# Kernel optimization log

Hardware: AMD Instinct MI355X
Metric: run time of the kernel (lower is better)

## Reference

```python
import jax, jax.numpy as jnp
import numpy as np

C, H, V, N, T = 256, 256, 10000, 8, 256


def _residual_mlp(x, w1, b1, w2, b2, w3, b3):
    # ResidualLayerOld: relu(lin2(relu(lin1(x)))) + x, then final Linear
    h = jax.nn.relu(x @ w1 + b1)
    h = jax.nn.relu(h @ w2 + b2) + x
    return h @ w3 + b3


def setup_inputs() -> dict:
    key = jax.random.key(0)
    ks = jax.random.split(key, 16)
    p = lambda k, shape: jax.random.normal(k, shape, jnp.float32) * 0.02
    return dict(
        text=jax.random.randint(ks[0], (N, T), 0, V),
        mask=jnp.ones((N, T), dtype=bool),
        lengths=jnp.full((N,), T - 1, dtype=jnp.int32),  # full-length sequences
        start_emb=jax.random.normal(ks[1], (C, H), jnp.float32),
        state_emb=jax.random.normal(ks[2], (C, H), jnp.float32),
        preterminal_emb=jax.random.normal(ks[3], (C, H), jnp.float32),
        start_w1=p(ks[4], (H, H)), start_b1=jnp.zeros((H,), jnp.float32),
        start_w2=p(ks[5], (H, H)), start_b2=jnp.zeros((H,), jnp.float32),
        start_w3=p(ks[6], (H, 1)), start_b3=jnp.zeros((1,), jnp.float32),
        trans_w1=p(ks[7], (H, H)), trans_b1=jnp.zeros((H,), jnp.float32),
        trans_w2=p(ks[8], (H, H)), trans_b2=jnp.zeros((H,), jnp.float32),
        trans_w3=p(ks[9], (H, C)), trans_b3=jnp.zeros((C,), jnp.float32),
        term_w1=p(ks[10], (H, H)), term_b1=jnp.zeros((H,), jnp.float32),
        term_w2=p(ks[11], (H, H)), term_b2=jnp.zeros((H,), jnp.float32),
        term_w3=p(ks[12], (H, V)), term_b3=jnp.zeros((V,), jnp.float32),
    )


def _score(text, mask, lengths,
           start_emb, state_emb, preterminal_emb,
           start_w1, start_b1, start_w2, start_b2, start_w3, start_b3,
           trans_w1, trans_b1, trans_w2, trans_b2, trans_w3, trans_b3,
           term_w1, term_b1, term_w2, term_b2, term_w3, term_b3):
    n, t = text.shape
    c = state_emb.shape[0]
    # start / transition / emission distributions (dropout_type == 'none')
    init = jax.nn.log_softmax(
        _residual_mlp(start_emb, start_w1, start_b1, start_w2, start_b2, start_w3, start_b3)[:, 0], -1)  # [C]
    trans = jax.nn.log_softmax(
        _residual_mlp(state_emb, trans_w1, trans_b1, trans_w2, trans_b2, trans_w3, trans_b3), -1)  # [C,C]
    log_em = jax.nn.log_softmax(
        _residual_mlp(preterminal_emb, term_w1, term_b1, term_w2, term_b2, term_w3, term_b3), -1)  # [C,V]
    obs = log_em.T[text]  # [N,T,C], log p(x_t | z=c)
    # torch_struct LinearChain.hmm edge potentials: phi[n,t,c_next,c_prev]
    phi = trans[None, None] + obs[:, 1:, :, None]  # [N,T-1,C,C]
    phi = phi.at[:, 0].add(init[None, None, :] + obs[:, 0][:, None, :])
    phi_t = jnp.swapaxes(phi, 0, 1)  # [T-1,N,C,C]

    def fwd_step(alpha, p):
        new = jax.nn.logsumexp(p + alpha[:, None, :], axis=-1)  # reduce over c_prev
        return new, new

    _, alphas = jax.lax.scan(fwd_step, jnp.zeros((n, c), phi.dtype), phi_t)  # [T-1,N,C]

    def bwd_step(beta, p):
        new = jax.nn.logsumexp(p + beta[:, :, None], axis=1)  # reduce over c_next
        return new, beta

    _, betas = jax.lax.scan(bwd_step, jnp.zeros((n, c), phi.dtype), phi_t, reverse=True)  # [T-1,N,C]

    alpha_prev = jnp.concatenate([jnp.zeros((1, n, c), phi.dtype), alphas[:-1]], 0)
    log_Z = jax.nn.logsumexp(alphas[-1], -1)  # [N]
    # edge posteriors
    log_m = alpha_prev[:, :, None, :] + phi_t + betas[:, :, :, None] - log_Z[None, :, None, None]
    marginals = jnp.swapaxes(jnp.exp(log_m), 0, 1)  # [N,T-1,C,C]

    evidence = jax.nn.logsumexp(alphas[lengths - 1, jnp.arange(n)], -1).sum()
    elbo = jnp.where(mask[:, 1:, None, None],
                     jax.lax.stop_gradient(marginals) * phi,
                     0.0).sum()
    return elbo, evidence


def reference(text, mask, lengths,
              start_emb, state_emb, preterminal_emb,
              start_w1, start_b1, start_w2, start_b2, start_w3, start_b3,
              trans_w1, trans_b1, trans_w2, trans_b2, trans_w3, trans_b3,
              term_w1, term_b1, term_w2, term_b2, term_w3, term_b3):
    elbo, evidence = _score(text, mask, lengths,
                            start_emb, state_emb, preterminal_emb,
                            start_w1, start_b1, start_w2, start_b2, start_w3, start_b3,
                            trans_w1, trans_b1, trans_w2, trans_b2, trans_w3, trans_b3,
                            term_w1, term_b1, term_w2, term_b2, term_w3, term_b3)
    return elbo, evidence
```

## Files before the change

kernel.cpp:

```cpp
#include <hip/hip_runtime.h>
#include <hip/hip_bf16.h>

#define C_ 256
#define H_ 256
#define V_ 10000
#define N_ 8
#define T_ 256
#define TM1_ 255
#define NB_ ((V_ + 31) / 32)

typedef _Float16 h2_t __attribute__((ext_vector_type(2)));
typedef _Float16 h4_t __attribute__((ext_vector_type(4)));
typedef _Float16 h8_t __attribute__((ext_vector_type(8)));
typedef float f4v __attribute__((ext_vector_type(4)));

__device__ __forceinline__ void bar_lgkm() {
  asm volatile("s_waitcnt lgkmcnt(0)\ns_barrier" ::: "memory");
}

__device__ __forceinline__ float wave_red_max(float v) {
#define DPP_MAX(ctrl) { int iv_ = __float_as_int(v); \
  int r_ = __builtin_amdgcn_update_dpp(iv_, iv_, ctrl, 0xF, 0xF, false); \
  v = fmaxf(v, __int_as_float(r_)); }
  DPP_MAX(0x111) DPP_MAX(0x112) DPP_MAX(0x114) DPP_MAX(0x118)
  DPP_MAX(0x142) DPP_MAX(0x143)
#undef DPP_MAX
  return __int_as_float(__builtin_amdgcn_readlane(__float_as_int(v), 63));
}
__device__ __forceinline__ float wave_red_sum(float v) {
#define DPP_ADD(ctrl) { \
  int r_ = __builtin_amdgcn_update_dpp(0, __float_as_int(v), ctrl, 0xF, 0xF, true); \
  v += __int_as_float(r_); }
  DPP_ADD(0x111) DPP_ADD(0x112) DPP_ADD(0x114) DPP_ADD(0x118)
  DPP_ADD(0x142) DPP_ADD(0x143)
#undef DPP_ADD
  return __int_as_float(__builtin_amdgcn_readlane(__float_as_int(v), 63));
}

__device__ __forceinline__ float block_allmax(float v, float* red) {
  v = wave_red_max(v);
  if ((threadIdx.x & 63) == 0) red[threadIdx.x >> 6] = v;
  __syncthreads();
  v = fmaxf(fmaxf(red[0], red[1]), fmaxf(red[2], red[3]));
  __syncthreads();
  return v;
}
__device__ __forceinline__ float block_allsum(float v, float* red) {
  v = wave_red_sum(v);
  if ((threadIdx.x & 63) == 0) red[threadIdx.x >> 6] = v;
  __syncthreads();
  v = (red[0] + red[1]) + (red[2] + red[3]);
  __syncthreads();
  return v;
}

__device__ __forceinline__ void mlp4(
    const float* __restrict__ emb,
    const float* __restrict__ w1, const float* __restrict__ b1,
    const float* __restrict__ w2, const float* __restrict__ b2,
    int r0, float (&e_s)[4][C_], float (&h_s)[4][C_], float (&h2_s)[4][C_]) {
  const int tid = threadIdx.x;
#pragma unroll
  for (int rr = 0; rr < 4; ++rr)
    e_s[rr][tid] = emb[(r0 + rr) * H_ + tid];
  __syncthreads();
  float bb = b1[tid];
  float a0 = bb, a1 = bb, a2 = bb, a3 = bb;
  for (int k4 = 0; k4 < H_ / 4; ++k4) {
    float4 e0 = ((const float4*)e_s[0])[k4];
    float4 e1 = ((const float4*)e_s[1])[k4];
    float4 e2 = ((const float4*)e_s[2])[k4];
    float4 e3 = ((const float4*)e_s[3])[k4];
    const float* wp = w1 + (k4 * 4) * H_ + tid;
    float wa = wp[0], wb = wp[H_], wc = wp[2 * H_], wd = wp[3 * H_];
    a0 = fmaf(e0.x, wa, a0); a0 = fmaf(e0.y, wb, a0);
    a0 = fmaf(e0.z, wc, a0); a0 = fmaf(e0.w, wd, a0);
    a1 = fmaf(e1.x, wa, a1); a1 = fmaf(e1.y, wb, a1);
    a1 = fmaf(e1.z, wc, a1); a1 = fmaf(e1.w, wd, a1);
    a2 = fmaf(e2.x, wa, a2); a2 = fmaf(e2.y, wb, a2);
    a2 = fmaf(e2.z, wc, a2); a2 = fmaf(e2.w, wd, a2);
    a3 = fmaf(e3.x, wa, a3); a3 = fmaf(e3.y, wb, a3);
    a3 = fmaf(e3.z, wc, a3); a3 = fmaf(e3.w, wd, a3);
  }
  h_s[0][tid] = fmaxf(a0, 0.f);
  h_s[1][tid] = fmaxf(a1, 0.f);
  h_s[2][tid] = fmaxf(a2, 0.f);
  h_s[3][tid] = fmaxf(a3, 0.f);
  __syncthreads();
  bb = b2[tid];
  a0 = bb; a1 = bb; a2 = bb; a3 = bb;
  for (int k4 = 0; k4 < H_ / 4; ++k4) {
    float4 e0 = ((const float4*)h_s[0])[k4];
    float4 e1 = ((const float4*)h_s[1])[k4];
    float4 e2 = ((const float4*)h_s[2])[k4];
    float4 e3 = ((const float4*)h_s[3])[k4];
    const float* wp = w2 + (k4 * 4) * H_ + tid;
    float wa = wp[0], wb = wp[H_], wc = wp[2 * H_], wd = wp[3 * H_];
    a0 = fmaf(e0.x, wa, a0); a0 = fmaf(e0.y, wb, a0);
    a0 = fmaf(e0.z, wc, a0); a0 = fmaf(e0.w, wd, a0);
    a1 = fmaf(e1.x, wa, a1); a1 = fmaf(e1.y, wb, a1);
    a1 = fmaf(e1.z, wc, a1); a1 = fmaf(e1.w, wd, a1);
    a2 = fmaf(e2.x, wa, a2); a2 = fmaf(e2.y, wb, a2);
    a2 = fmaf(e2.z, wc, a2); a2 = fmaf(e2.w, wd, a2);
    a3 = fmaf(e3.x, wa, a3); a3 = fmaf(e3.y, wb, a3);
    a3 = fmaf(e3.z, wc, a3); a3 = fmaf(e3.w, wd, a3);
  }
  h2_s[0][tid] = fmaxf(a0, 0.f) + e_s[0][tid];
  h2_s[1][tid] = fmaxf(a1, 0.f) + e_s[1][tid];
  h2_s[2][tid] = fmaxf(a2, 0.f) + e_s[2][tid];
  h2_s[3][tid] = fmaxf(a3, 0.f) + e_s[3][tid];
  __syncthreads();
}

__global__ __launch_bounds__(256) void k_start(
    const float* __restrict__ emb, const float* __restrict__ w1,
    const float* __restrict__ b1, const float* __restrict__ w2,
    const float* __restrict__ b2, const float* __restrict__ w3,
    const float* __restrict__ b3, float* __restrict__ slogit) {
  __shared__ __align__(16) float e_s[4][C_], h_s[4][C_], h2_s[4][C_];
  __shared__ float red[4];
  const int r0 = blockIdx.x * 4;
  const int tid = threadIdx.x;
  mlp4(emb, w1, b1, w2, b2, r0, e_s, h_s, h2_s);
  float w3v = w3[tid];
  float s0 = block_allsum(h2_s[0][tid] * w3v, red);
  float s1 = block_allsum(h2_s[1][tid] * w3v, red);
  float s2 = block_allsum(h2_s[2][tid] * w3v, red);
  float s3 = block_allsum(h2_s[3][tid] * w3v, red);
  if (tid == 0) {
    float bb = b3[0];
    slogit[r0 + 0] = s0 + bb;
    slogit[r0 + 1] = s1 + bb;
    slogit[r0 + 2] = s2 + bb;
    slogit[r0 + 3] = s3 + bb;
  }
}

__global__ void k_init(const float* __restrict__ slogit, float* __restrict__ initv) {
  __shared__ float red[4];
  const int tid = threadIdx.x;
  float x = slogit[tid];
  float m = block_allmax(x, red);
  float se = block_allsum(__expf(x - m), red);
  initv[tid] = x - m - __logf(se);
}

__global__ __launch_bounds__(256) void k_trans(
    const float* __restrict__ emb, const float* __restrict__ w1,
    const float* __restrict__ b1, const float* __restrict__ w2,
    const float* __restrict__ b2, const float* __restrict__ w3,
    const float* __restrict__ b3, float* __restrict__ Pf,
    float* __restrict__ PLf, float* __restrict__ PTf,
    _Float16* __restrict__ P_h, _Float16* __restrict__ PT_h) {
  __shared__ __align__(16) float e_s[4][C_], h_s[4][C_], h2_s[4][C_];
  __shared__ float red[4];
  const int r0 = blockIdx.x * 4;
  const int tid = threadIdx.x;
  mlp4(emb, w1, b1, w2, b2, r0, e_s, h_s, h2_s);
  float lb = b3[tid];
  float l0 = lb, l1 = lb, l2 = lb, l3 = lb;
  for (int k4 = 0; k4 < H_ / 4; ++k4) {
    float4 e0 = ((const float4*)h2_s[0])[k4];
    float4 e1 = ((const float4*)h2_s[1])[k4];
    float4 e2 = ((const float4*)h2_s[2])[k4];
    float4 e3 = ((const float4*)h2_s[3])[k4];
    const float* wp = w3 + (k4 * 4) * C_ + tid;
    float wa = wp[0], wb = wp[C_], wc = wp[2 * C_], wd = wp[3 * C_];
    l0 = fmaf(e0.x, wa, l0); l0 = fmaf(e0.y, wb, l0);
    l0 = fmaf(e0.z, wc, l0); l0 = fmaf(e0.w, wd, l0);
    l1 = fmaf(e1.x, wa, l1); l1 = fmaf(e1.y, wb, l1);
    l1 = fmaf(e1.z, wc, l1); l1 = fmaf(e1.w, wd, l1);
    l2 = fmaf(e2.x, wa, l2); l2 = fmaf(e2.y, wb, l2);
    l2 = fmaf(e2.z, wc, l2); l2 = fmaf(e2.w, wd, l2);
    l3 = fmaf(e3.x, wa, l3); l3 = fmaf(e3.y, wb, l3);
    l3 = fmaf(e3.z, wc, l3); l3 = fmaf(e3.w, wd, l3);
  }
  float lg[4] = {l0, l1, l2, l3};
#pragma unroll
  for (int rr = 0; rr < 4; ++rr) {
    float m = block_allmax(lg[rr], red);
    float e = __expf(lg[rr] - m);
    float se = block_allsum(e, red);
    float p = e / se;
    float tv = lg[rr] - m - __logf(se);
    const int r = r0 + rr;
    Pf[r * C_ + tid] = p;
    PLf[r * C_ + tid] = p * tv;
    PTf[tid * C_ + r] = p;
    P_h[r * C_ + tid] = (_Float16)p;
    PT_h[tid * C_ + r] = (_Float16)p;
  }
}

__global__ __launch_bounds__(256) void k_term_mlp(
    const float* __restrict__ emb, const float* __restrict__ w1,
    const float* __restrict__ b1, const float* __restrict__ w2,
    const float* __restrict__ b2, float* __restrict__ H2,
    float* __restrict__ H2T) {
  __shared__ __align__(16) float e_s[4][C_], h_s[4][C_], h2_s[4][C_];
  const int r0 = blockIdx.x * 4;
  const int tid = threadIdx.x;
  mlp4(emb, w1, b1, w2, b2, r0, e_s, h_s, h2_s);
#pragma unroll
  for (int rr = 0; rr < 4; ++rr) {
    const int r = r0 + rr;
    float v = h2_s[rr][tid];
    H2[r * H_ + tid] = v;
    H2T[tid * C_ + r] = v;
  }
}

__global__ __launch_bounds__(256) void k_term_stats(
    const float* __restrict__ H2, const float* __restrict__ w3,
    const float* __restrict__ b3, float* __restrict__ partm,
    float* __restrict__ parts) {
  __shared__ __align__(16) float w3_s[H_][32];
  __shared__ float b3_s[32];
  const int v0 = blockIdx.x * 32;
  const int tid = threadIdx.x;
  const int ncols = min(32, V_ - v0);
  for (int idx = tid; idx < H_ * 32; idx += 256) {
    int k = idx >> 5, c = idx & 31;
    w3_s[k][c] = (c < ncols) ? w3[k * V_ + v0 + c] : 0.f;
  }
  if (tid < 32) b3_s[tid] = (tid < ncols) ? b3[v0 + tid] : 0.f;
  __syncthreads();
  float acc[32];
#pragma unroll
  for (int c = 0; c < 32; ++c) acc[c] = 0.f;
  const float4* hq = (const float4*)(H2 + tid * H_);
  for (int k4 = 0; k4 < H_ / 4; ++k4) {
    float4 h = hq[k4];
    float hk[4];
    *(float4*)hk = h;
#pragma unroll
    for (int kk = 0; kk < 4; ++kk) {
      float hv = hk[kk];
      const int k = k4 * 4 + kk;
      const float4* wq = (const float4*)(&w3_s[k][0]);
#pragma unroll
      for (int c4 = 0; c4 < 8; ++c4) {
        float4 w = wq[c4];
        acc[c4 * 4 + 0] = fmaf(hv, w.x, acc[c4 * 4 + 0]);
        acc[c4 * 4 + 1] = fmaf(hv, w.y, acc[c4 * 4 + 1]);
        acc[c4 * 4 + 2] = fmaf(hv, w.z, acc[c4 * 4 + 2]);
        acc[c4 * 4 + 3] = fmaf(hv, w.w, acc[c4 * 4 + 3]);
      }
    }
  }
  float m = -1e30f;
#pragma unroll
  for (int c = 0; c < 32; ++c) {
    acc[c] += b3_s[c];
    if (c < ncols) m = fmaxf(m, acc[c]);
  }
  float se = 0.f;
#pragma unroll
  for (int c = 0; c < 32; ++c)
    if (c < ncols) se += __expf(acc[c] - m);
  partm[blockIdx.x * C_ + tid] = m;
  parts[blockIdx.x * C_ + tid] = se;
}

__global__ void k_denom(const float* __restrict__ partm,
                        const float* __restrict__ parts,
                        float* __restrict__ denom) {
  const int r = threadIdx.x;
  float m = -1e30f;
  for (int b = 0; b < NB_; ++b) m = fmaxf(m, partm[b * C_ + r]);
  float s = 0.f;
  for (int b = 0; b < NB_; ++b)
    s += parts[b * C_ + r] * __expf(partm[b * C_ + r] - m);
  denom[r] = m + __logf(s);
}

__global__ __launch_bounds__(256) void k_obs2(
    const int* __restrict__ text, const float* __restrict__ H2T,
    const float* __restrict__ w3, const float* __restrict__ b3,
    const float* __restrict__ denom, float* __restrict__ EOBS,
    float* __restrict__ Karr) {
  __shared__ __align__(16) float w_s[H_][8];
  __shared__ float redm[4][8];
  const int c = threadIdx.x;
  const int wid = c >> 6;
  const int lane = c & 63;
  const int base = blockIdx.x * 8;
  int tok[8];
#pragma unroll
  for (int i = 0; i < 8; ++i) tok[i] = text[base + i];
  float wtmp[8];
#pragma unroll
  for (int i = 0; i < 8; ++i) wtmp[i] = w3[c * V_ + tok[i]];
  float b3t[8];
#pragma unroll
  for (int i = 0; i < 8; ++i) b3t[i] = b3[tok[i]];
#pragma unroll
  for (int i = 0; i < 8; ++i) w_s[c][i] = wtmp[i];
  __syncthreads();
  float acc[8];
#pragma unroll
  for (int i = 0; i < 8; ++i) acc[i] = 0.f;
  for (int k4 = 0; k4 < H_ / 4; ++k4) {
    float hv[4];
#pragma unroll
    for (int kk = 0; kk < 4; ++kk) hv[kk] = H2T[(k4 * 4 + kk) * C_ + c];
#pragma unroll
    for (int kk = 0; kk < 4; ++kk) {
      const float4* wq = (const float4*)(&w_s[k4 * 4 + kk][0]);
      float4 wa = wq[0], wb = wq[1];
      acc[0] = fmaf(hv[kk], wa.x, acc[0]);
      acc[1] = fmaf(hv[kk], wa.y, acc[1]);
      acc[2] = fmaf(hv[kk], wa.z, acc[2]);
      acc[3] = fmaf(hv[kk], wa.w, acc[3]);
      acc[4] = fmaf(hv[kk], wb.x, acc[4]);
      acc[5] = fmaf(hv[kk], wb.y, acc[5]);
      acc[6] = fmaf(hv[kk], wb.z, acc[6]);
      acc[7] = fmaf(hv[kk], wb.w, acc[7]);
    }
  }
  float dn = denom[c];
  float obsv[8];
#pragma unroll
  for (int i = 0; i < 8; ++i) obsv[i] = acc[i] + b3t[i] - dn;
#pragma unroll
  for (int i = 0; i < 8; ++i) {
    float wm = wave_red_max(obsv[i]);
    if (lane == 0) redm[wid][i] = wm;
  }
  __syncthreads();
#pragma unroll
  for (int i = 0; i < 8; ++i) {
    float Ki = fmaxf(fmaxf(redm[0][i], redm[1][i]),
                     fmaxf(redm[2][i], redm[3][i]));
    EOBS[(base + i) * C_ + c] = __expf(obsv[i] - Ki);
    if (c == 0) Karr[base + i] = Ki;
  }
}

__global__ __launch_bounds__(256, 1) void k_scan4(
    const _Float16* __restrict__ P_h, const _Float16* __restrict__ PT_h,
    const float* __restrict__ initv, const float* __restrict__ EOBS,
    const float* __restrict__ Karr, float* __restrict__ AL,
    float* __restrict__ BL, float* __restrict__ CC, float* __restrict__ DD,
    float* __restrict__ LOGZ) {
  __shared__ __align__(16) _Float16 ubuf[2][C_];
  __shared__ float red[4];
  const int tid = threadIdx.x;
  const int wave = tid >> 6;
  const int lane = tid & 63;
  const int quad = lane >> 4;
  const int nn16 = lane & 15;
  const bool bwd = blockIdx.x >= N_;
  const int n = blockIdx.x & (N_ - 1);
  const _Float16* __restrict__ M = bwd ? PT_h : P_h;

  h8_t afrag[4][8];
#pragma unroll
  for (int mt = 0; mt < 4; ++mt) {
    const _Float16* rp = M + (size_t)((wave << 6) + (mt << 4) + nn16) * C_ + (quad << 3);
#pragma unroll
    for (int kt = 0; kt < 8; ++kt)
      afrag[mt][kt] = *(const h8_t*)(rp + (kt << 5));
  }
  const int stb = (wave << 6) + (quad << 2);

  if (!bwd) {
    float K0 = Karr[n * T_];
    f4v x0[4];
    float lmax = -1e30f;
#pragma unroll
    for (int mt = 0; mt < 4; ++mt) {
      const int st0 = stb + (mt << 4);
      f4v iv = *(const f4v*)(initv + st0);
      f4v e0 = *(const f4v*)(EOBS + (size_t)(n * T_) * C_ + st0);
#pragma unroll
      for (int r = 0; r < 4; ++r) {
        x0[mt][r] = iv[r] + __logf(e0[r]) + K0;
        lmax = fmaxf(lmax, x0[mt][r]);
      }
    }
    float wm = wave_red_max(lmax);
    if (lane == 0) red[wave] = wm;
    __syncthreads();
    float m0 = fmaxf(fmaxf(red[0], red[1]), fmaxf(red[2], red[3]));
    __syncthreads();
    float Cacc = m0;
    f4v uval[4];
#pragma unroll
    for (int mt = 0; mt < 4; ++mt) {
      const int st0 = stb + (mt << 4);
#pragma unroll
      for (int r = 0; r < 4; ++r) uval[mt][r] = __expf(x0[mt][r] - m0);
      if (nn16 == 0) {
        h4_t p;
#pragma unroll
        for (int r = 0; r < 4; ++r) p[r] = (_Float16)uval[mt][r];
        *(h4_t*)(&ubuf[0][st0]) = p;
        *(f4v*)(AL + (size_t)(0 * N_ + n) * C_ + st0) = uval[mt];
      }
    }
    if (tid == 0) CC[0 * N_ + n] = Cacc;
    float invm = 1.f, logm = 0.f;
    f4v eo_nx[4];
#pragma unroll
    for (int mt = 0; mt < 4; ++mt)
      eo_nx[mt] = *(const f4v*)(EOBS + (size_t)(n * T_ + 1) * C_ + stb + (mt << 4));
    float K_nx = Karr[n * T_ + 1];
    __syncthreads();

#pragma unroll 1
    for (int t = 0; t < TM1_; ++t) {
      const int cur = t & 1, nxt = cur ^ 1;
      f4v eo_pf[4];
      float K_pf = 0.f;
      if (t + 2 < T_) {
#pragma unroll
        for (int mt = 0; mt < 4; ++mt)
          eo_pf[mt] = *(const f4v*)(EOBS + (size_t)(n * T_ + t + 2) * C_ + stb + (mt << 4));
        K_pf = Karr[n * T_ + t + 2];
      }
      h8_t bf[8];
#pragma unroll
      for (int kt = 0; kt < 8; ++kt)
        bf[kt] = *(const h8_t*)(&ubuf[cur][(kt << 5) + (quad << 3)]);
      f4v acc[4];
#pragma unroll
      for (int mt = 0; mt < 4; ++mt) acc[mt] = (f4v){0.f, 0.f, 0.f, 0.f};
#pragma unroll
      for (int kt = 0; kt < 8; ++kt) {
#pragma unroll
        for (int mt = 0; mt < 4; ++mt)
          acc[mt] = __builtin_amdgcn_mfma_f32_16x16x32_f16(afrag[mt][kt], bf[kt], acc[mt], 0, 0, 0);
      }
      float lmx = -1e30f;
#pragma unroll
      for (int mt = 0; mt < 4; ++mt) {
#pragma unroll
        for (int r = 0; r < 4; ++r) {
          float u = acc[mt][r] * invm * eo_nx[mt][r];
          uval[mt][r] = u;
          lmx = fmaxf(lmx, u);
        }
      }
      Cacc += K_nx + logm;
      const bool resc = (t & 3) == 3;
      if (resc) {
        float wmm = wave_red_max(lmx);
        if (lane == 0) red[wave] = wmm;
      }
      if (nn16 == 0) {
#pragma unroll
        for (int mt = 0; mt < 4; ++mt) {
          const int st0 = stb + (mt << 4);
          h4_t p;
#pragma unroll
          for (int r = 0; r < 4; ++r) p[r] = (_Float16)uval[mt][r];
          *(h4_t*)(&ubuf[nxt][st0]) = p;
          *(f4v*)(AL + (size_t)((t + 1) * N_ + n) * C_ + st0) = uval[mt];
        }
      }
      if (tid == 0) CC[(t + 1) * N_ + n] = Cacc;
      bar_lgkm();
      if (resc) {
        float m = fmaxf(fmaxf(red[0], red[1]), fmaxf(red[2], red[3]));
        m = fmaxf(m, 1e-30f);
        invm = 1.f / m;
        logm = __logf(m);
      } else { invm = 1.f; logm = 0.f; }
#pragma unroll
      for (int mt = 0; mt < 4; ++mt) eo_nx[mt] = eo_pf[mt];
      K_nx = K_pf;
    }
    float s = 0.f;
#pragma unroll
    for (int mt = 0; mt < 4; ++mt)
      s += (uval[mt][0] + uval[mt][1]) + (uval[mt][2] + uval[mt][3]);
    s = wave_red_sum(s);
    if (lane == 0) red[wave] = s;
    __syncthreads();
    float S = ((red[0] + red[1]) + (red[2] + red[3])) * (1.f / 16.f);
    if (tid == 0) LOGZ[n] = __logf(S) + Cacc;
  } else {
    float Dacc = 0.f;
    f4v vval[4];
#pragma unroll
    for (int mt = 0; mt < 4; ++mt) {
      const int st0 = stb + (mt << 4);
      vval[mt] = *(const f4v*)(EOBS + ((size_t)n * T_ + TM1_) * C_ + st0);
      if (nn16 == 0) {
        h4_t p;
#pragma unroll
        for (int r = 0; r < 4; ++r) p[r] = (_Float16)vval[mt][r];
        *(h4_t*)(&ubuf[0][st0]) = p;
        f4v one = (f4v){1.f, 1.f, 1.f, 1.f};
        *(f4v*)(BL + (size_t)((TM1_ - 1) * N_ + n) * C_ + st0) = one;
      }
    }
    if (tid == 0) DD[(TM1_ - 1) * N_ + n] = 0.f;
    float K_nx = Karr[n * T_ + TM1_];
    f4v eo_nx[4];
#pragma unroll
    for (int mt = 0; mt < 4; ++mt)
      eo_nx[mt] = *(const f4v*)(EOBS + (size_t)(n * T_ + TM1_ - 1) * C_ + stb + (mt << 4));
    __syncthreads();

#pragma unroll 1
    for (int it = 0, t = TM1_ - 2; t >= 0; --t, ++it) {
      const int cur = it & 1, nxt = cur ^ 1;
      f4v eo_pf[4];
      float K_pf = 0.f;
      if (t >= 1) {
#pragma unroll
        for (int mt = 0; mt < 4; ++mt)
          eo_pf[mt] = *(const f4v*)(EOBS + (size_t)(n * T_ + t) * C_ + stb + (mt << 4));
        K_pf = Karr[n * T_ + t + 1];
      }
      float invm = 1.f, logm = 0.f;
      if ((it & 3) == 3) {
        float m = fmaxf(fmaxf(red[0], red[1]), fmaxf(red[2], red[3]));
        m = fmaxf(m, 1e-30f);
        invm = 1.f / m;
        logm = __logf(m);
      }
      h8_t bf[8];
#pragma unroll
      for (int kt = 0; kt < 8; ++kt)
        bf[kt] = *(const h8_t*)(&ubuf[cur][(kt << 5) + (quad << 3)]);
      f4v acc[4];
#pragma unroll
      for (int mt = 0; mt < 4; ++mt) acc[mt] = (f4v){0.f, 0.f, 0.f, 0.f};
#pragma unroll
      for (int kt = 0; kt < 8; ++kt) {
#pragma unroll
        for (int mt = 0; mt < 4; ++mt)
          acc[mt] = __builtin_amdgcn_mfma_f32_16x16x32_f16(afrag[mt][kt], bf[kt], acc[mt], 0, 0, 0);
      }
      Dacc += K_nx + logm;
      float lmx = -1e30f;
      f4v blv[4];
#pragma unroll
      for (int mt = 0; mt < 4; ++mt) {
#pragma unroll
        for (int r = 0; r < 4; ++r) {
          float b = acc[mt][r] * invm;
          blv[mt][r] = b;
          float v = b * eo_nx[mt][r];
          vval[mt][r] = v;
          lmx = fmaxf(lmx, v);
        }
      }
      if (((it + 1) & 3) == 3) {
        float wmm = wave_red_max(lmx);
        if (lane == 0) red[wave] = wmm;
      }
      if (nn16 == 0) {
#pragma unroll
        for (int mt = 0; mt < 4; ++mt) {
          const int st0 = stb + (mt << 4);
          h4_t p;
#pragma unroll
          for (int r = 0; r < 4; ++r) p[r] = (_Float16)vval[mt][r];
          *(h4_t*)(&ubuf[nxt][st0]) = p;
          *(f4v*)(BL + (size_t)(t * N_ + n) * C_ + st0) = blv[mt];
        }
      }
      if (tid == 0) DD[t * N_ + n] = Dacc;
      bar_lgkm();
#pragma unroll
      for (int mt = 0; mt < 4; ++mt) eo_nx[mt] = eo_pf[mt];
      K_nx = K_pf;
    }
  }
}

__global__ __launch_bounds__(256) void k_elbo(
    const float* __restrict__ Pf, const float* __restrict__ PLf,
    const float* __restrict__ PTf, const float* __restrict__ AL,
    const float* __restrict__ BL, const float* __restrict__ CC,
    const float* __restrict__ DD, const float* __restrict__ EOBS,
    const float* __restrict__ Karr, const float* __restrict__ LOGZ,
    float* __restrict__ out) {
  __shared__ __align__(16) float A_s[N_][C_];
  __shared__ __align__(16) float B_s[N_][C_];
  __shared__ float red[4];
  const int t = blockIdx.x;
  const int c = threadIdx.x;
  if (t == 0 && c == 0) {
    float s = 0.f;
#pragma unroll
    for (int nn = 0; nn < N_; ++nn) s += LOGZ[nn];
    out[1] = s;
  }
  float sc[N_], Kv[N_], cc[N_];
#pragma unroll
  for (int nn = 0; nn < N_; ++nn) {
    A_s[nn][c] = AL[(t * N_ + nn) * C_ + c];
    Kv[nn] = Karr[nn * T_ + t + 1];
    cc[nn] = CC[t * N_ + nn];
    sc[nn] = __expf(cc[nn] + DD[t * N_ + nn] + Kv[nn] - LOGZ[nn]);
  }
  __syncthreads();
  float accPA[N_], accPL[N_];
#pragma unroll
  for (int nn = 0; nn < N_; ++nn) { accPA[nn] = 0.f; accPL[nn] = 0.f; }
  const float4* pr = (const float4*)(Pf + c * C_);
  const float4* plr = (const float4*)(PLf + c * C_);
  for (int j = 0; j < C_ / 4; ++j) {
    float4 p = pr[j];
    float4 pl = plr[j];
#pragma unroll
    for (int nn = 0; nn < N_; ++nn) {
      float4 a = ((const float4*)A_s[nn])[j];
      accPA[nn] += p.x * a.x + p.y * a.y + p.z * a.z + p.w * a.w;
      accPL[nn] += pl.x * a.x + pl.y * a.y + pl.z * a.z + pl.w * a.w;
    }
  }
  float contrib = 0.f;
  float Bv[N_];
#pragma unroll
  for (int nn = 0; nn < N_; ++nn) {
    float eo = EOBS[(nn * T_ + t + 1) * C_ + c];
    float ob = __logf(eo) + Kv[nn];
    float B = eo * BL[(t * N_ + nn) * C_ + c] * sc[nn];
    Bv[nn] = B;
    contrib += B * fmaf(ob, accPA[nn], accPL[nn]);
  }
  if (t == 0) {
#pragma unroll
    for (int nn = 0; nn < N_; ++nn) B_s[nn][c] = Bv[nn];
    __syncthreads();
    const float4* ptq = (const float4*)(PTf + c * C_);
    float accPT[N_];
#pragma unroll
    for (int nn = 0; nn < N_; ++nn) accPT[nn] = 0.f;
    for (int j = 0; j < C_ / 4; ++j) {
      float4 p = ptq[j];
#pragma unroll
      for (int nn = 0; nn < N_; ++nn) {
        float4 b = ((const float4*)B_s[nn])[j];
        accPT[nn] += p.x * b.x + p.y * b.y + p.z * b.z + p.w * b.w;
      }
    }
#pragma unroll
    for (int nn = 0; nn < N_; ++nn) {
      float a0v = A_s[nn][c];
      if (a0v > 0.f)
        contrib += a0v * (__logf(a0v) + cc[nn]) * accPT[nn];
    }
  }
  contrib = wave_red_sum(contrib);
  if ((c & 63) == 0) red[c >> 6] = contrib;
  __syncthreads();
  if (c == 0) atomicAdd(out, (red[0] + red[1]) + (red[2] + red[3]));
}

extern "C" void kernel_launch(void* const* d_in, const int* in_sizes, int n_in,
                              void* d_out, int out_size, void* d_ws, size_t ws_size,
                              hipStream_t stream) {
  (void)in_sizes; (void)n_in; (void)out_size; (void)ws_size;
  const int* text = (const int*)d_in[0];
  const float* start_emb = (const float*)d_in[3];
  const float* state_emb = (const float*)d_in[4];
  const float* pre_emb   = (const float*)d_in[5];
  const float* sw1 = (const float*)d_in[6];  const float* sb1 = (const float*)d_in[7];
  const float* sw2 = (const float*)d_in[8];  const float* sb2 = (const float*)d_in[9];
  const float* sw3 = (const float*)d_in[10]; const float* sb3 = (const float*)d_in[11];
  const float* tw1 = (const float*)d_in[12]; const float* tb1 = (const float*)d_in[13];
  const float* tw2 = (const float*)d_in[14]; const float* tb2 = (const float*)d_in[15];
  const float* tw3 = (const float*)d_in[16]; const float* tb3 = (const float*)d_in[17];
  const float* ew1 = (const float*)d_in[18]; const float* eb1 = (const float*)d_in[19];
  const float* ew2 = (const float*)d_in[20]; const float* eb2 = (const float*)d_in[21];
  const float* ew3 = (const float*)d_in[22]; const float* eb3 = (const float*)d_in[23];
  float* out = (float*)d_out;

  char* p = (char*)d_ws;
  auto alloc = [&](size_t bytes) -> char* {
    char* r = p;
    p += (bytes + 255) & ~(size_t)255;
    return r;
  };
  float* slogit = (float*)alloc(C_ * 4);
  float* initv  = (float*)alloc(C_ * 4);
  float* denom  = (float*)alloc(C_ * 4);
  float* LOGZ   = (float*)alloc(N_ * 4);
  float* Pf     = (float*)alloc(C_ * C_ * 4);
  float* PLf    = (float*)alloc(C_ * C_ * 4);
  float* PTf    = (float*)alloc(C_ * C_ * 4);
  _Float16* P_h  = (_Float16*)alloc(C_ * C_ * 2);
  _Float16* PT_h = (_Float16*)alloc(C_ * C_ * 2);
  float* H2    = (float*)alloc(C_ * H_ * 4);
  float* H2T   = (float*)alloc(C_ * H_ * 4);
  float* partm = (float*)alloc(NB_ * C_ * 4);
  float* parts = (float*)alloc(NB_ * C_ * 4);
  float* EOBS  = (float*)alloc((size_t)N_ * T_ * C_ * 4);
  float* Karr  = (float*)alloc((size_t)N_ * T_ * 4);
  float* AL    = (float*)alloc((size_t)T_ * N_ * C_ * 4);
  float* BL    = (float*)alloc((size_t)TM1_ * N_ * C_ * 4);
  float* CC    = (float*)alloc((size_t)T_ * N_ * 4);
  float* DD    = (float*)alloc((size_t)TM1_ * N_ * 4);

  hipMemsetAsync(d_out, 0, 2 * sizeof(float), stream);

  k_start<<<dim3(C_ / 4), dim3(256), 0, stream>>>(start_emb, sw1, sb1, sw2, sb2, sw3, sb3, slogit);
  k_init<<<dim3(1), dim3(256), 0, stream>>>(slogit, initv);
  k_trans<<<dim3(C_ / 4), dim3(256), 0, stream>>>(state_emb, tw1, tb1, tw2, tb2, tw3, tb3,
                                                  Pf, PLf, PTf, P_h, PT_h);
  k_term_mlp<<<dim3(C_ / 4), dim3(256), 0, stream>>>(pre_emb, ew1, eb1, ew2, eb2, H2, H2T);
  k_term_stats<<<dim3(NB_), dim3(256), 0, stream>>>(H2, ew3, eb3, partm, parts);
  k_denom<<<dim3(1), dim3(256), 0, stream>>>(partm, parts, denom);
  k_obs2<<<dim3(N_ * T_ / 8), dim3(256), 0, stream>>>(text, H2T, ew3, eb3, denom, EOBS, Karr);
  k_scan4<<<dim3(2 * N_), dim3(256), 0, stream>>>(P_h, PT_h, initv, EOBS, Karr,
                                                  AL, BL, CC, DD, LOGZ);
  k_elbo<<<dim3(TM1_), dim3(256), 0, stream>>>(Pf, PLf, PTf, AL, BL, CC, DD,
                                               EOBS, Karr, LOGZ, out);
}
```

Before: 550.4 us.

## Split HMM scan across eight waves with deeper emission prefetch

After: 517.0 us. -6.1%, faster.

```diff
diff --git a/kernel.cpp b/kernel.cpp
--- a/kernel.cpp
+++ b/kernel.cpp
@@ -8,6 +8,7 @@
 #define T_ 256
 #define TM1_ 255
 #define NB_ ((V_ + 31) / 32)
+#define SW_ 8
 
 typedef _Float16 h2_t __attribute__((ext_vector_type(2)));
 typedef _Float16 h4_t __attribute__((ext_vector_type(4)));
@@ -337,16 +338,16 @@
   }
 }
 
-__global__ __launch_bounds__(256, 1) void k_scan4(
+__global__ __launch_bounds__(512, 2) void k_scan5(
     const _Float16* __restrict__ P_h, const _Float16* __restrict__ PT_h,
     const float* __restrict__ initv, const float* __restrict__ EOBS,
     const float* __restrict__ Karr, float* __restrict__ AL,
     float* __restrict__ BL, float* __restrict__ CC, float* __restrict__ DD,
     float* __restrict__ LOGZ) {
   __shared__ __align__(16) _Float16 ubuf[2][C_];
-  __shared__ float red[4];
+  __shared__ __align__(16) float red[SW_];
   const int tid = threadIdx.x;
-  const int wave = tid >> 6;
+  const int w = tid >> 6;
   const int lane = tid & 63;
   const int quad = lane >> 4;
   const int nn16 = lane & 15;
@@ -354,91 +355,96 @@
   const int n = blockIdx.x & (N_ - 1);
   const _Float16* __restrict__ M = bwd ? PT_h : P_h;
 
-  h8_t afrag[4][8];
-#pragma unroll
-  for (int mt = 0; mt < 4; ++mt) {
-    const _Float16* rp = M + (size_t)((wave << 6) + (mt << 4) + nn16) * C_ + (quad << 3);
+  h8_t afrag[2][8];
+#pragma unroll
+  for (int m = 0; m < 2; ++m) {
+    const _Float16* rp = M + (size_t)((w << 5) + (m << 4) + nn16) * C_ + (quad << 3);
 #pragma unroll
     for (int kt = 0; kt < 8; ++kt)
-      afrag[mt][kt] = *(const h8_t*)(rp + (kt << 5));
-  }
-  const int stb = (wave << 6) + (quad << 2);
+      afrag[m][kt] = *(const h8_t*)(rp + (kt << 5));
+  }
+  const int stb = (w << 5) + (quad << 2);
 
   if (!bwd) {
     float K0 = Karr[n * T_];
-    f4v x0[4];
+    f4v x0[2];
     float lmax = -1e30f;
 #pragma unroll
-    for (int mt = 0; mt < 4; ++mt) {
-      const int st0 = stb + (mt << 4);
+    for (int m = 0; m < 2; ++m) {
+      const int st0 = stb + (m << 4);
       f4v iv = *(const f4v*)(initv + st0);
       f4v e0 = *(const f4v*)(EOBS + (size_t)(n * T_) * C_ + st0);
 #pragma unroll
       for (int r = 0; r < 4; ++r) {
-        x0[mt][r] = iv[r] + __logf(e0[r]) + K0;
-        lmax = fmaxf(lmax, x0[mt][r]);
-      }
-    }
-    float wm = wave_red_max(lmax);
-    if (lane == 0) red[wave] = wm;
+        x0[m][r] = iv[r] + __logf(e0[r]) + K0;
+        lmax = fmaxf(lmax, x0[m][r]);
+      }
+    }
+    float wmx = wave_red_max(lmax);
+    if (lane == 0) red[w] = wmx;
     __syncthreads();
-    float m0 = fmaxf(fmaxf(red[0], red[1]), fmaxf(red[2], red[3]));
+    f4v rr0 = *(const f4v*)&red[0];
+    f4v rr1 = *(const f4v*)&red[4];
+    float m0 = fmaxf(fmaxf(fmaxf(rr0[0], rr0[1]), fmaxf(rr0[2], rr0[3])),
+                     fmaxf(fmaxf(rr1[0], rr1[1]), fmaxf(rr1[2], rr1[3])));
     __syncthreads();
     float Cacc = m0;
-    f4v uval[4];
-#pragma unroll
-    for (int mt = 0; mt < 4; ++mt) {
-      const int st0 = stb + (mt << 4);
-#pragma unroll
-      for (int r = 0; r < 4; ++r) uval[mt][r] = __expf(x0[mt][r] - m0);
+    f4v uval[2];
+#pragma unroll
+    for (int m = 0; m < 2; ++m) {
+      const int st0 = stb + (m << 4);
+#pragma unroll
+      for (int r = 0; r < 4; ++r) uval[m][r] = __expf(x0[m][r] - m0);
       if (nn16 == 0) {
         h4_t p;
 #pragma unroll
-        for (int r = 0; r < 4; ++r) p[r] = (_Float16)uval[mt][r];
+        for (int r = 0; r < 4; ++r) p[r] = (_Float16)uval[m][r];
         *(h4_t*)(&ubuf[0][st0]) = p;
-        *(f4v*)(AL + (size_t)(0 * N_ + n) * C_ + st0) = uval[mt];
+        *(f4v*)(AL + (size_t)(0 * N_ + n) * C_ + st0) = uval[m];
       }
     }
     if (tid == 0) CC[0 * N_ + n] = Cacc;
     float invm = 1.f, logm = 0.f;
-    f4v eo_nx[4];
-#pragma unroll
-    for (int mt = 0; mt < 4; ++mt)
-      eo_nx[mt] = *(const f4v*)(EOBS + (size_t)(n * T_ + 1) * C_ + stb + (mt << 4));
+    f4v eo_nx[2], eo_p1[2];
+#pragma unroll
+    for (int m = 0; m < 2; ++m) {
+      eo_nx[m] = *(const f4v*)(EOBS + (size_t)(n * T_ + 1) * C_ + stb + (m << 4));
+      eo_p1[m] = *(const f4v*)(EOBS + (size_t)(n * T_ + 2) * C_ + stb + (m << 4));
+    }
     float K_nx = Karr[n * T_ + 1];
+    float K_p1 = Karr[n * T_ + 2];
     __syncthreads();
 
 #pragma unroll 1
     for (int t = 0; t < TM1_; ++t) {
       const int cur = t & 1, nxt = cur ^ 1;
-      f4v eo_pf[4];
-      float K_pf = 0.f;
-      if (t + 2 < T_) {
-#pragma unroll
-        for (int mt = 0; mt < 4; ++mt)
-          eo_pf[mt] = *(const f4v*)(EOBS + (size_t)(n * T_ + t + 2) * C_ + stb + (mt << 4));
-        K_pf = Karr[n * T_ + t + 2];
+      f4v eo_p2[2];
+      float K_p2 = 0.f;
+      if (t + 3 < T_) {
+#pragma unroll
+        for (int m = 0; m < 2; ++m)
+          eo_p2[m] = *(const f4v*)(EOBS + (size_t)(n * T_ + t + 3) * C_ + stb + (m << 4));
+        K_p2 = Karr[n * T_ + t + 3];
       }
       h8_t bf[8];
 #pragma unroll
       for (int kt = 0; kt < 8; ++kt)
         bf[kt] = *(const h8_t*)(&ubuf[cur][(kt << 5) + (quad << 3)]);
-      f4v acc[4];
-#pragma unroll
-      for (int mt = 0; mt < 4; ++mt) acc[mt] = (f4v){0.f, 0.f, 0.f, 0.f};
+      f4v acc[2];
+      acc[0] = (f4v){0.f, 0.f, 0.f, 0.f};
+      acc[1] = (f4v){0.f, 0.f, 0.f, 0.f};
 #pragma unroll
       for (int kt = 0; kt < 8; ++kt) {
-#pragma unroll
-        for (int mt = 0; mt < 4; ++mt)
-          acc[mt] = __builtin_amdgcn_mfma_f32_16x16x32_f16(afrag[mt][kt], bf[kt], acc[mt], 0, 0, 0);
+        acc[0] = __builtin_amdgcn_mfma_f32_16x16x32_f16(afrag[0][kt], bf[kt], acc[0], 0, 0, 0);
+        acc[1] = __builtin_amdgcn_mfma_f32_16x16x32_f16(afrag[1][kt], bf[kt], acc[1], 0, 0, 0);
       }
       float lmx = -1e30f;
 #pragma unroll
-      for (int mt = 0; mt < 4; ++mt) {
+      for (int m = 0; m < 2; ++m) {
 #pragma unroll
         for (int r = 0; r < 4; ++r) {
-          float u = acc[mt][r] * invm * eo_nx[mt][r];
-          uval[mt][r] = u;
+          float u = acc[m][r] * invm * eo_nx[m][r];
+          uval[m][r] = u;
           lmx = fmaxf(lmx, u);
         }
       }
@@ -446,51 +452,57 @@
       const bool resc = (t & 3) == 3;
       if (resc) {
         float wmm = wave_red_max(lmx);
-        if (lane == 0) red[wave] = wmm;
+        if (lane == 0) red[w] = wmm;
       }
       if (nn16 == 0) {
 #pragma unroll
-        for (int mt = 0; mt < 4; ++mt) {
-          const int st0 = stb + (mt << 4);
+        for (int m = 0; m < 2; ++m) {
+          const int st0 = stb + (m << 4);
           h4_t p;
 #pragma unroll
-          for (int r = 0; r < 4; ++r) p[r] = (_Float16)uval[mt][r];
+          for (int r = 0; r < 4; ++r) p[r] = (_Float16)uval[m][r];
           *(h4_t*)(&ubuf[nxt][st0]) = p;
-          *(f4v*)(AL + (size_t)((t + 1) * N_ + n) * C_ + st0) = uval[mt];
+          *(f4v*)(AL + (size_t)((t + 1) * N_ + n) * C_ + st0) = uval[m];
         }
       }
       if (tid == 0) CC[(t + 1) * N_ + n] = Cacc;
       bar_lgkm();
       if (resc) {
-        float m = fmaxf(fmaxf(red[0], red[1]), fmaxf(red[2], red[3]));
-        m = fmaxf(m, 1e-30f);
-        invm = 1.f / m;
-        logm = __logf(m);
+        f4v q0 = *(const f4v*)&red[0];
+        f4v q1 = *(const f4v*)&red[4];
+        float mm = fmaxf(fmaxf(fmaxf(q0[0], q0[1]), fmaxf(q0[2], q0[3])),
+                         fmaxf(fmaxf(q1[0], q1[1]), fmaxf(q1[2], q1[3])));
+        mm = fmaxf(mm, 1e-30f);
+        invm = 1.f / mm;
+        logm = __logf(mm);
       } else { invm = 1.f; logm = 0.f; }
 #pragma unroll
-      for (int mt = 0; mt < 4; ++mt) eo_nx[mt] = eo_pf[mt];
-      K_nx = K_pf;
+      for (int m = 0; m < 2; ++m) { eo_nx[m] = eo_p1[m]; eo_p1[m] = eo_p2[m]; }
+      K_nx = K_p1; K_p1 = K_p2;
     }
     float s = 0.f;
 #pragma unroll
-    for (int mt = 0; mt < 4; ++mt)
-      s += (uval[mt][0] + uval[mt][1]) + (uval[mt][2] + uval[mt][3]);
+    for (int m = 0; m < 2; ++m)
+      s += (uval[m][0] + uval[m][1]) + (uval[m][2] + uval[m][3]);
     s = wave_red_sum(s);
-    if (lane == 0) red[wave] = s;
+    if (lane == 0) red[w] = s;
     __syncthreads();
-    float S = ((red[0] + red[1]) + (red[2] + red[3])) * (1.f / 16.f);
-    if (tid == 0) LOGZ[n] = __logf(S) + Cacc;
+    if (tid == 0) {
+      float S = ((red[0] + red[1]) + (red[2] + red[3])) +
+                ((red[4] + red[5]) + (red[6] + red[7]));
+      LOGZ[n] = __logf(S * (1.f / 16.f)) + Cacc;
+    }
   } else {
     float Dacc = 0.f;
-    f4v vval[4];
-#pragma unroll
-    for (int mt = 0; mt < 4; ++mt) {
-      const int st0 = stb + (mt << 4);
-      vval[mt] = *(const f4v*)(EOBS + ((size_t)n * T_ + TM1_) * C_ + st0);
+    f4v vval[2];
+#pragma unroll
+    for (int m = 0; m < 2; ++m) {
+      const int st0 = stb + (m << 4);
+      vval[m] = *(const f4v*)(EOBS + ((size_t)n * T_ + TM1_) * C_ + st0);
       if (nn16 == 0) {
         h4_t p;
 #pragma unroll
-        for (int r = 0; r < 4; ++r) p[r] = (_Float16)vval[mt][r];
+        for (int r = 0; r < 4; ++r) p[r] = (_Float16)vval[m][r];
         *(h4_t*)(&ubuf[0][st0]) = p;
         f4v one = (f4v){1.f, 1.f, 1.f, 1.f};
         *(f4v*)(BL + (size_t)((TM1_ - 1) * N_ + n) * C_ + st0) = one;
@@ -498,77 +510,82 @@
     }
     if (tid == 0) DD[(TM1_ - 1) * N_ + n] = 0.f;
     float K_nx = Karr[n * T_ + TM1_];
-    f4v eo_nx[4];
-#pragma unroll
-    for (int mt = 0; mt < 4; ++mt)
-      eo_nx[mt] = *(const f4v*)(EOBS + (size_t)(n * T_ + TM1_ - 1) * C_ + stb + (mt << 4));
+    float K_p1 = Karr[n * T_ + TM1_ - 1];
+    f4v eo_nx[2], eo_p1[2];
+#pragma unroll
+    for (int m = 0; m < 2; ++m) {
+      eo_nx[m] = *(const f4v*)(EOBS + (size_t)(n * T_ + TM1_ - 1) * C_ + stb + (m << 4));
+      eo_p1[m] = *(const f4v*)(EOBS + (size_t)(n * T_ + TM1_ - 2) * C_ + stb + (m << 4));
+    }
+    float invm = 1.f, logm = 0.f;
     __syncthreads();
 
 #pragma unroll 1
     for (int it = 0, t = TM1_ - 2; t >= 0; --t, ++it) {
       const int cur = it & 1, nxt = cur ^ 1;
-      f4v eo_pf[4];
-      float K_pf = 0.f;
-      if (t >= 1) {
-#pragma unroll
-        for (int mt = 0; mt < 4; ++mt)
-          eo_pf[mt] = *(const f4v*)(EOBS + (size_t)(n * T_ + t) * C_ + stb + (mt << 4));
-        K_pf = Karr[n * T_ + t + 1];
-      }
-      float invm = 1.f, logm = 0.f;
-      if ((it & 3) == 3) {
-        float m = fmaxf(fmaxf(red[0], red[1]), fmaxf(red[2], red[3]));
-        m = fmaxf(m, 1e-30f);
-        invm = 1.f / m;
-        logm = __logf(m);
+      f4v eo_p2[2];
+      float K_p2 = 0.f;
+      if (t >= 2) {
+#pragma unroll
+        for (int m = 0; m < 2; ++m)
+          eo_p2[m] = *(const f4v*)(EOBS + (size_t)(n * T_ + t - 1) * C_ + stb + (m << 4));
+        K_p2 = Karr[n * T_ + t];
       }
       h8_t bf[8];
 #pragma unroll
       for (int kt = 0; kt < 8; ++kt)
         bf[kt] = *(const h8_t*)(&ubuf[cur][(kt << 5) + (quad << 3)]);
-      f4v acc[4];
-#pragma unroll
-      for (int mt = 0; mt < 4; ++mt) acc[mt] = (f4v){0.f, 0.f, 0.f, 0.f};
+      f4v acc[2];
+      acc[0] = (f4v){0.f, 0.f, 0.f, 0.f};
+      acc[1] = (f4v){0.f, 0.f, 0.f, 0.f};
 #pragma unroll
       for (int kt = 0; kt < 8; ++kt) {
-#pragma unroll
-        for (int mt = 0; mt < 4; ++mt)
-          acc[mt] = __builtin_amdgcn_mfma_f32_16x16x32_f16(afrag[mt][kt], bf[kt], acc[mt], 0, 0, 0);
+        acc[0] = __builtin_amdgcn_mfma_f32_16x16x32_f16(afrag[0][kt], bf[kt], acc[0], 0, 0, 0);
+        acc[1] = __builtin_amdgcn_mfma_f32_16x16x32_f16(afrag[1][kt], bf[kt], acc[1], 0, 0, 0);
       }
       Dacc += K_nx + logm;
       float lmx = -1e30f;
-      f4v blv[4];
-#pragma unroll
-      for (int mt = 0; mt < 4; ++mt) {
+      f4v blv[2];
+#pragma unroll
+      for (int m = 0; m < 2; ++m) {
 #pragma unroll
         for (int r = 0; r < 4; ++r) {
-          float b = acc[mt][r] * invm;
-          blv[mt][r] = b;
-          float v = b * eo_nx[mt][r];
-          vval[mt][r] = v;
+          float b = acc[m][r] * invm;
+          blv[m][r] = b;
+          float v = b * eo_nx[m][r];
+          vval[m][r] = v;
           lmx = fmaxf(lmx, v);
         }
       }
       if (((it + 1) & 3) == 3) {
         float wmm = wave_red_max(lmx);
-        if (lane == 0) red[wave] = wmm;
+        if (lane == 0) red[w] = wmm;
       }
       if (nn16 == 0) {
 #pragma unroll
-        for (int mt = 0; mt < 4; ++mt) {
-          const int st0 = stb + (mt << 4);
+        for (int m = 0; m < 2; ++m) {
+          const int st0 = stb + (m << 4);
           h4_t p;
 #pragma unroll
-          for (int r = 0; r < 4; ++r) p[r] = (_Float16)vval[mt][r];
+          for (int r = 0; r < 4; ++r) p[r] = (_Float16)vval[m][r];
           *(h4_t*)(&ubuf[nxt][st0]) = p;
-          *(f4v*)(BL + (size_t)(t * N_ + n) * C_ + st0) = blv[mt];
+          *(f4v*)(BL + (size_t)(t * N_ + n) * C_ + st0) = blv[m];
         }
       }
       if (tid == 0) DD[t * N_ + n] = Dacc;
       bar_lgkm();
-#pragma unroll
-      for (int mt = 0; mt < 4; ++mt) eo_nx[mt] = eo_pf[mt];
-      K_nx = K_pf;
+      if (((it + 1) & 3) == 3) {
+        f4v q0 = *(const f4v*)&red[0];
+        f4v q1 = *(const f4v*)&red[4];
+        float mm = fmaxf(fmaxf(fmaxf(q0[0], q0[1]), fmaxf(q0[2], q0[3])),
+                         fmaxf(fmaxf(q1[0], q1[1]), fmaxf(q1[2], q1[3])));
+        mm = fmaxf(mm, 1e-30f);
+        invm = 1.f / mm;
+        logm = __logf(mm);
+      } else { invm = 1.f; logm = 0.f; }
+#pragma unroll
+      for (int m = 0; m < 2; ++m) { eo_nx[m] = eo_p1[m]; eo_p1[m] = eo_p2[m]; }
+      K_nx = K_p1; K_p1 = K_p2;
     }
   }
 }
@@ -709,7 +726,7 @@
   k_term_stats<<<dim3(NB_), dim3(256), 0, stream>>>(H2, ew3, eb3, partm, parts);
   k_denom<<<dim3(1), dim3(256), 0, stream>>>(partm, parts, denom);
   k_obs2<<<dim3(N_ * T_ / 8), dim3(256), 0, stream>>>(text, H2T, ew3, eb3, denom, EOBS, Karr);
-  k_scan4<<<dim3(2 * N_), dim3(256), 0, stream>>>(P_h, PT_h, initv, EOBS, Karr,
+  k_scan5<<<dim3(2 * N_), dim3(512), 0, stream>>>(P_h, PT_h, initv, EOBS, Karr,
                                                   AL, BL, CC, DD, LOGZ);
   k_elbo<<<dim3(TM1_), dim3(256), 0, stream>>>(Pf, PLf, PTf, AL, BL, CC, DD,
                                                EOBS, Karr, LOGZ, out);
```
